# Optimization experiments

Measured on AMD Instinct MI355X. Metric: run time of the kernel, lower is better.

Reference implementation:

```python
import jax, jax.numpy as jnp
import numpy as np

B, S, D, H = 2, 2048, 1024, 16
DK = D // H
EPS = 1e-5


def setup_inputs() -> dict:
    key = jax.random.key(0)
    ks = jax.random.split(key, 6)
    std = (2.0 / (D + D)) ** 0.5
    return {
        "x": jax.random.normal(ks[0], (B, S, D), dtype=jnp.float32),
        "W_Q": jax.random.normal(ks[1], (D, D), dtype=jnp.float32) * std,
        "W_K": jax.random.normal(ks[2], (D, D), dtype=jnp.float32) * std,
        "W_V": jax.random.normal(ks[3], (D, D), dtype=jnp.float32) * std,
        "W_O": jax.random.normal(ks[4], (D, D), dtype=jnp.float32) * std,
        "gain": jnp.ones((D,), dtype=jnp.float32),
        "positions": jnp.arange(S, dtype=jnp.int64 if jax.config.jax_enable_x64 else jnp.int32),
        "theta": 10000,
        "max_seq_len": 2048,
    }


def rmsnorm(x, gain):
    xf = x.astype(jnp.float32)
    rms = jnp.sqrt(jnp.mean(xf * xf, axis=-1, keepdims=True) + EPS)
    return ((xf / rms) * gain).astype(x.dtype)


def apply_rope(x, sin, cos):
    # x: [..., seq, dk]; sin/cos: [seq, dk//2] broadcast over leading dims
    x_even = x[..., 0::2]
    x_odd = x[..., 1::2]
    r_even = x_even * cos - x_odd * sin
    r_odd = x_odd * cos + x_even * sin
    return jnp.stack([r_even, r_odd], axis=-1).reshape(x.shape)


def reference(x, W_Q, W_K, W_V, W_O, gain, positions, theta, max_seq_len):
    seq_len = x.shape[-2]
    Q = jnp.einsum('od,bsd->bso', W_Q, x)
    K = jnp.einsum('od,bsd->bso', W_K, x)
    V = jnp.einsum('od,bsd->bso', W_V, x)
    # RMSNorm over full d_model BEFORE head split (as in original)
    Q = rmsnorm(Q, gain)
    K = rmsnorm(K, gain)
    # split heads: [b, h, s, dk]
    Q = Q.reshape(*Q.shape[:-1], H, DK).swapaxes(-3, -2)
    K = K.reshape(*K.shape[:-1], H, DK).swapaxes(-3, -2)
    V = V.reshape(*V.shape[:-1], H, DK).swapaxes(-3, -2)
    # RoPE tables
    exponents = 2.0 * jnp.arange(DK // 2, dtype=jnp.float32) / DK
    inv_freq = 1.0 / (jnp.float32(theta) ** exponents)
    angles = positions.astype(jnp.float32)[:, None] * inv_freq[None, :]  # [S, DK//2]
    sin, cos = jnp.sin(angles), jnp.cos(angles)
    Q = apply_rope(Q, sin, cos)
    K = apply_rope(K, sin, cos)
    # causal attention
    scores = jnp.einsum('bhqd,bhkd->bhqk', Q, K) / jnp.sqrt(jnp.float32(DK))
    causal = jnp.tril(jnp.ones((seq_len, seq_len), dtype=bool))
    scores = jnp.where(causal, scores, -jnp.inf)
    attn = jax.nn.softmax(scores, axis=-1)
    out = jnp.einsum('bhqk,bhkd->bhqd', attn, V)
    out = out.swapaxes(-3, -2).reshape(*x.shape[:-1], D)
    return jnp.einsum('of,bsf->bso', W_O, out)
```

## Files before the change

### kernel.cpp

```cpp
#include <hip/hip_runtime.h>
#include <hip/hip_bf16.h>

typedef __attribute__((ext_vector_type(8))) __bf16 bf16x8;
typedef __attribute__((ext_vector_type(4))) __bf16 bf16x4;
typedef __attribute__((ext_vector_type(4))) float  f32x4;
typedef __attribute__((ext_vector_type(4))) short  s16x4;

#define S_LEN 2048
#define D_DIM 1024
#define NH    16
#define GK    1024
#define GN    1024

__device__ __forceinline__ float fast_exp2(float x) {
#if __has_builtin(__builtin_amdgcn_exp2f)
  return __builtin_amdgcn_exp2f(x);
#else
  return exp2f(x);
#endif
}

__device__ __forceinline__ f32x4 mfma16(bf16x4 a, bf16x4 b, f32x4 c) {
#if __has_builtin(__builtin_amdgcn_mfma_f32_16x16x16_bf16)
  return __builtin_amdgcn_mfma_f32_16x16x16_bf16(a, b, c, 0, 0, 0);
#else
  return __builtin_amdgcn_mfma_f32_16x16x16bf16_1k(
      __builtin_bit_cast(s16x4, a), __builtin_bit_cast(s16x4, b), c, 0, 0, 0);
#endif
}

__device__ __forceinline__ void gld_lds16(const void* g, void* l) {
  __builtin_amdgcn_global_load_lds(
      (const __attribute__((address_space(1))) unsigned int*)g,
      (__attribute__((address_space(3))) unsigned int*)l, 16, 0, 0);
}

__global__ __launch_bounds__(256) void cast_all(
    const float* __restrict__ x,  const float* __restrict__ wq, const float* __restrict__ wk,
    const float* __restrict__ wv, const float* __restrict__ wo,
    __bf16* __restrict__ xb, __bf16* __restrict__ wqb, __bf16* __restrict__ wkb,
    __bf16* __restrict__ wvb, __bf16* __restrict__ wob)
{
  const int NTOT = 2 << 20;
  for (int i = blockIdx.x * 256 + threadIdx.x; i < NTOT; i += 1024 * 256) {
    const float* s; __bf16* d; int off;
    if (i < (1 << 20)) { s = x; d = xb; off = i; }
    else {
      const int j = i - (1 << 20);
      const int r = j >> 18; off = j & ((1 << 18) - 1);
      s = (r == 0) ? wq : (r == 1) ? wk : (r == 2) ? wv : wo;
      d = (r == 0) ? wqb : (r == 1) ? wkb : (r == 2) ? wvb : wob;
    }
    float4 v = ((const float4*)s)[off];
    bf16x4 o = { (__bf16)v.x, (__bf16)v.y, (__bf16)v.z, (__bf16)v.w };
    ((bf16x4*)d)[off] = o;
  }
}

__global__ __launch_bounds__(256, 3) void gemm_qkv(
    const __bf16* __restrict__ A,
    const __bf16* __restrict__ W0, const __bf16* __restrict__ W1, const __bf16* __restrict__ W2,
    __bf16* __restrict__ C0, __bf16* __restrict__ C1, __bf16* __restrict__ VtOut)
{
  const int bid = blockIdx.x;
  const int e = bid & 7, mg = e >> 1, ng = e & 1;
  const int q = bid >> 3;
  const int mt = mg * 8 + (q & 7);
  const int nt = ng * 12 + (q >> 3);
  const int mode = nt >> 3;
  const int m0 = mt * 128;
  const int n0 = (nt & 7) * 128;
  const __bf16* Wm = (mode == 0) ? W0 : (mode == 1) ? W1 : W2;

  __shared__ __align__(16) __bf16 As[128 * 64];
  __shared__ __align__(16) __bf16 Bs[128 * 64];

  const int tid  = threadIdx.x;
  const int lane = tid & 63;
  const int w    = tid >> 6;
  const int wr   = w >> 1, wc = w & 1;
  const int lm   = lane & 15, qd = lane >> 4;

  const __bf16* ap[4]; int loA[4];
  #pragma unroll
  for (int j = 0; j < 4; j++) {
    const int c = tid + 256 * j;
    const int r = c >> 3, cpos = c & 7;
    ap[j] = A + (size_t)(m0 + r) * GK + (cpos ^ (r & 7)) * 8;
    loA[j] = c * 8;
  }
  const __bf16* bp[4]; int loB[4];
  #pragma unroll
  for (int j = 0; j < 4; j++) {
    const int c = tid + 256 * j;
    const int r = c >> 3, cpos = c & 7;
    bp[j] = Wm + (size_t)(n0 + r) * GK + (cpos ^ (r & 7)) * 8;
    loB[j] = c * 8;
  }

  const int sw = lm & 7;

  f32x4 zero = {0.f, 0.f, 0.f, 0.f};
  f32x4 acc[4][4];
  #pragma unroll
  for (int i = 0; i < 4; i++)
    #pragma unroll
    for (int j = 0; j < 4; j++) acc[i][j] = zero;

  for (int k0 = 0; k0 < GK; k0 += 64) {
    #pragma unroll
    for (int j = 0; j < 4; j++) gld_lds16(ap[j] + k0, &As[loA[j]]);
    #pragma unroll
    for (int j = 0; j < 4; j++) gld_lds16(bp[j] + k0, &Bs[loB[j]]);
    __syncthreads();
    #pragma unroll
    for (int half = 0; half < 2; half++) {
      const int cph = ((qd + 4 * half) ^ sw) * 8;
      bf16x8 af[4], bfv[4];
      #pragma unroll
      for (int i = 0; i < 4; i++) af[i]  = *(const bf16x8*)&As[(wr * 64 + i * 16 + lm) * 64 + cph];
      #pragma unroll
      for (int j = 0; j < 4; j++) bfv[j] = *(const bf16x8*)&Bs[(wc * 64 + j * 16 + lm) * 64 + cph];
      #pragma unroll
      for (int i = 0; i < 4; i++)
        #pragma unroll
        for (int j = 0; j < 4; j++)
          acc[i][j] = __builtin_amdgcn_mfma_f32_16x16x32_bf16(af[i], bfv[j], acc[i][j], 0, 0, 0);
    }
    __syncthreads();
  }

  if (mode < 2) {
    __bf16* C = (mode == 0) ? C0 : C1;
    #pragma unroll
    for (int i = 0; i < 4; i++) {
      const int row = m0 + wr * 64 + i * 16 + qd * 4;
      #pragma unroll
      for (int j = 0; j < 4; j++) {
        const int col = n0 + wc * 64 + j * 16 + lm;
        #pragma unroll
        for (int r = 0; r < 4; r++)
          C[(size_t)(row + r) * GN + col] = (__bf16)acc[i][j][r];
      }
    }
  } else {
    #pragma unroll
    for (int i = 0; i < 4; i++) {
      const int row = m0 + wr * 64 + i * 16 + qd * 4;
      const int b = row >> 11, s = row & (S_LEN - 1);
      #pragma unroll
      for (int j = 0; j < 4; j++) {
        const int col = n0 + wc * 64 + j * 16 + lm;
        const int h = col >> 6, d = col & 63;
        bf16x4 o = { (__bf16)acc[i][j][0], (__bf16)acc[i][j][1],
                     (__bf16)acc[i][j][2], (__bf16)acc[i][j][3] };
        *(bf16x4*)(VtOut + (((size_t)(b * NH + h) * 64 + d) * S_LEN + s)) = o;
      }
    }
  }
}

__global__ __launch_bounds__(256, 2) void gemm_out64(
    const __bf16* __restrict__ A, const __bf16* __restrict__ Wm, float* __restrict__ C)
{
  const int bid = blockIdx.x;
  const int e = bid & 7, mg = e >> 1, ng = e & 1;
  const int q = bid >> 3;
  const int m0 = (mg * 16 + (q & 15)) * 64;
  const int n0 = (ng * 4 + (q >> 4)) * 128;

  __shared__ __align__(16) __bf16 As[2][64 * 64];
  __shared__ __align__(16) __bf16 Bs[2][128 * 64];

  const int tid  = threadIdx.x;
  const int lane = tid & 63;
  const int w    = tid >> 6;
  const int wr   = w >> 1, wc = w & 1;
  const int lm   = lane & 15, qd = lane >> 4;

  const __bf16* ap[2]; int loA[2];
  #pragma unroll
  for (int j = 0; j < 2; j++) {
    const int c = tid + 256 * j;
    const int r = c >> 3, cpos = c & 7;
    ap[j] = A + (size_t)(m0 + r) * GK + (cpos ^ (r & 7)) * 8;
    loA[j] = c * 8;
  }
  const __bf16* bp[4]; int loB[4];
  #pragma unroll
  for (int j = 0; j < 4; j++) {
    const int c = tid + 256 * j;
    const int r = c >> 3, cpos = c & 7;
    bp[j] = Wm + (size_t)(n0 + r) * GK + (cpos ^ (r & 7)) * 8;
    loB[j] = c * 8;
  }

  const int sw = lm & 7;

  auto stage = [&](int buf, int k0) {
    #pragma unroll
    for (int j = 0; j < 2; j++) gld_lds16(ap[j] + k0, &As[buf][loA[j]]);
    #pragma unroll
    for (int j = 0; j < 4; j++) gld_lds16(bp[j] + k0, &Bs[buf][loB[j]]);
  };

  f32x4 zero = {0.f, 0.f, 0.f, 0.f};
  f32x4 acc[2][4];
  #pragma unroll
  for (int i = 0; i < 2; i++)
    #pragma unroll
    for (int j = 0; j < 4; j++) acc[i][j] = zero;

  stage(0, 0);

  for (int kt = 0; kt < 16; ++kt) {
    const int cur = kt & 1;
    __syncthreads();
    if (kt < 15) stage(cur ^ 1, (kt + 1) * 64);
    #pragma unroll
    for (int half = 0; half < 2; half++) {
      const int cph = ((qd + 4 * half) ^ sw) * 8;
      bf16x8 af[2], bfv[4];
      #pragma unroll
      for (int i = 0; i < 2; i++) af[i]  = *(const bf16x8*)&As[cur][(wr * 32 + i * 16 + lm) * 64 + cph];
      #pragma unroll
      for (int j = 0; j < 4; j++) bfv[j] = *(const bf16x8*)&Bs[cur][(wc * 64 + j * 16 + lm) * 64 + cph];
      #pragma unroll
      for (int i = 0; i < 2; i++)
        #pragma unroll
        for (int j = 0; j < 4; j++)
          acc[i][j] = __builtin_amdgcn_mfma_f32_16x16x32_bf16(af[i], bfv[j], acc[i][j], 0, 0, 0);
    }
  }

  #pragma unroll
  for (int i = 0; i < 2; i++) {
    const int row = m0 + wr * 32 + i * 16 + qd * 4;
    #pragma unroll
    for (int j = 0; j < 4; j++) {
      const int col = n0 + wc * 64 + j * 16 + lm;
      #pragma unroll
      for (int r = 0; r < 4; r++)
        C[(size_t)(row + r) * GN + col] = acc[i][j][r];
    }
  }
}

__global__ __launch_bounds__(256) void norm_rope(
    const __bf16* __restrict__ Qf, const __bf16* __restrict__ Kf,
    const float* __restrict__ gain, const int* __restrict__ positions,
    const int* __restrict__ theta_p,
    __bf16* __restrict__ Qh, __bf16* __restrict__ Kh)
{
  const int row = blockIdx.x;
  const int s = row & (S_LEN - 1), b = row >> 11;
  const int t = threadIdx.x, d0 = t * 4;

  const bf16x4 qv = *(const bf16x4*)(Qf + (size_t)row * D_DIM + d0);
  const bf16x4 kv = *(const bf16x4*)(Kf + (size_t)row * D_DIM + d0);
  const float q0 = (float)qv[0], q1 = (float)qv[1], q2 = (float)qv[2], q3 = (float)qv[3];
  const float k0 = (float)kv[0], k1 = (float)kv[1], k2 = (float)kv[2], k3 = (float)kv[3];

  float sq = q0 * q0 + q1 * q1 + q2 * q2 + q3 * q3;
  float sk = k0 * k0 + k1 * k1 + k2 * k2 + k3 * k3;
  #pragma unroll
  for (int off = 32; off; off >>= 1) { sq += __shfl_xor(sq, off); sk += __shfl_xor(sk, off); }
  __shared__ float red[8];
  const int lane = t & 63, wv = t >> 6;
  if (lane == 0) { red[wv] = sq; red[4 + wv] = sk; }
  __syncthreads();
  sq = red[0] + red[1] + red[2] + red[3];
  sk = red[4] + red[5] + red[6] + red[7];
  const float SC2 = 0.125f * 1.44269504089f;
  const float invq = rsqrtf(sq * (1.0f / 1024.0f) + 1e-5f) * SC2;
  const float invk = rsqrtf(sk * (1.0f / 1024.0f) + 1e-5f);

  const float4 g = *(const float4*)(gain + d0);
  const float qn0 = q0 * invq * g.x, qn1 = q1 * invq * g.y;
  const float qn2 = q2 * invq * g.z, qn3 = q3 * invq * g.w;
  const float kn0 = k0 * invk * g.x, kn1 = k1 * invk * g.y;
  const float kn2 = k2 * invk * g.z, kn3 = k3 * invk * g.w;

  const float pos = (float)positions[s];
  const float th  = (float)theta_p[0];
  const int idx = d0 & 63, h = d0 >> 6, p0 = idx >> 1;
  const float lg32 = __log2f(th) * (1.0f / 32.0f);
  const float f0 = fast_exp2(-(float)p0 * lg32);
  const float f1 = fast_exp2(-(float)(p0 + 1) * lg32);
  float s0, cc0, s1, cc1;
  __sincosf(pos * f0, &s0, &cc0);
  __sincosf(pos * f1, &s1, &cc1);

  const float qe0 = qn0 * cc0 - qn1 * s0, qo0 = qn1 * cc0 + qn0 * s0;
  const float qe1 = qn2 * cc1 - qn3 * s1, qo1 = qn3 * cc1 + qn2 * s1;
  const float ke0 = kn0 * cc0 - kn1 * s0, ko0 = kn1 * cc0 + kn0 * s0;
  const float ke1 = kn2 * cc1 - kn3 * s1, ko1 = kn3 * cc1 + kn2 * s1;

  const size_t obase = ((size_t)((b * NH + h) * S_LEN + s)) * 64 + idx;
  bf16x4 qo = { (__bf16)qe0, (__bf16)qo0, (__bf16)qe1, (__bf16)qo1 };
  bf16x4 ko = { (__bf16)ke0, (__bf16)ko0, (__bf16)ke1, (__bf16)ko1 };
  *(bf16x4*)(Qh + obase) = qo;
  *(bf16x4*)(Kh + obase) = ko;
}

__global__ __launch_bounds__(256) void attn_fwd(
    const __bf16* __restrict__ Qh, const __bf16* __restrict__ Kh,
    const __bf16* __restrict__ Vt, __bf16* __restrict__ Ob)
{
  const int bid = blockIdx.x;
  const int g   = bid >> 5;
  const int gj = g & 7, gs = g >> 3;
  const int qt  = gs ? gj : 15 - gj;
  const int rr  = bid & 31;
  const int bh  = (rr & 7) * 4 + (rr >> 3);
  const int tid = threadIdx.x, lane = tid & 63, w = tid >> 6;
  const int lm = lane & 15, qd = lane >> 4;

  __shared__ __align__(16) __bf16 smem[8192 + 8192];
  __bf16* Ks = smem;
  __bf16* Vs = smem + 8192;

  const int qA = qt * 128 + w * 32 + lm;
  const int qB = qA + 16;
  const size_t qbase = (size_t)bh * S_LEN * 64;
  const bf16x8 aqA0 = *(const bf16x8*)(Qh + qbase + (size_t)qA * 64 + qd * 8);
  const bf16x8 aqA1 = *(const bf16x8*)(Qh + qbase + (size_t)qA * 64 + 32 + qd * 8);
  const bf16x8 aqB0 = *(const bf16x8*)(Qh + qbase + (size_t)qB * 64 + qd * 8);
  const bf16x8 aqB1 = *(const bf16x8*)(Qh + qbase + (size_t)qB * 64 + 32 + qd * 8);

  const __bf16* Kb = Kh + (size_t)bh * S_LEN * 64;
  const __bf16* Vb = Vt + (size_t)bh * 64 * S_LEN;
  const int c0 = tid, c1 = 256 + tid;
  const int kr0 = c0 >> 3, kr1 = c1 >> 3;
  const int kg0 = ((c0 & 7) ^ (kr0 & 7)) * 8;
  const int kg1 = ((c1 & 7) ^ (kr1 & 7)) * 8;
  const int cpA = (qd ^ (lm & 7)) * 8;
  const int cpB = cpA ^ 32;

  auto stage = [&](int buf, int k0) {
    __bf16* Kd = Ks + buf * 4096;
    __bf16* Vd = Vs + buf * 4096;
    gld_lds16(Kb + (size_t)(k0 + kr0) * 64 + kg0, &Kd[c0 * 8]);
    gld_lds16(Kb + (size_t)(k0 + kr1) * 64 + kg1, &Kd[c1 * 8]);
    gld_lds16(Vb + (size_t)kr0 * S_LEN + k0 + kg0, &Vd[c0 * 8]);
    gld_lds16(Vb + (size_t)kr1 * S_LEN + k0 + kg1, &Vd[c1 * 8]);
  };

  f32x4 zero = {0.f, 0.f, 0.f, 0.f};
  f32x4 laccA = zero, laccB = zero;
  f32x4 oA[4], oB[4];
  #pragma unroll
  for (int jb = 0; jb < 4; jb++) { oA[jb] = zero; oB[jb] = zero; }

  bf16x4 ones4;
  #pragma unroll
  for (int i = 0; i < 4; i++) ones4[i] = (__bf16)1.0f;

  const int NT = 2 * qt + 2;
  const int wq0 = qt * 128 + w * 32;

  stage(0, 0);

  for (int kt = 0; kt < NT; ++kt) {
    const int cur = kt & 1;
    __syncthreads();
    if (kt < NT - 1) stage(cur ^ 1, (kt + 1) * 64);

    const int k0 = kt * 64;
    if (k0 > wq0 + 31) continue;

    const __bf16* Kc = Ks + cur * 4096;
    const __bf16* Vc = Vs + cur * 4096;
    const bool needMask = (k0 + 63 > wq0);

    bf16x4 pfA[4], pfB[4];
    #pragma unroll
    for (int kb = 0; kb < 4; kb++) {
      const int krow = (kb * 16 + lm) * 64;
      const bf16x8 ak0 = *(const bf16x8*)&Kc[krow + cpA];
      const bf16x8 ak1 = *(const bf16x8*)&Kc[krow + cpB];
      f32x4 scA = zero, scB = zero;
      scA = __builtin_amdgcn_mfma_f32_16x16x32_bf16(ak0, aqA0, scA, 0, 0, 0);
      scB = __builtin_amdgcn_mfma_f32_16x16x32_bf16(ak0, aqB0, scB, 0, 0, 0);
      scA = __builtin_amdgcn_mfma_f32_16x16x32_bf16(ak1, aqA1, scA, 0, 0, 0);
      scB = __builtin_amdgcn_mfma_f32_16x16x32_bf16(ak1, aqB1, scB, 0, 0, 0);
      float pA[4], pB[4];
      if (needMask) {
        const int keyb = k0 + kb * 16 + qd * 4;
        #pragma unroll
        for (int r = 0; r < 4; r++) {
          pA[r] = (keyb + r <= qA) ? fast_exp2(scA[r]) : 0.f;
          pB[r] = (keyb + r <= qB) ? fast_exp2(scB[r]) : 0.f;
        }
      } else {
        #pragma unroll
        for (int r = 0; r < 4; r++) { pA[r] = fast_exp2(scA[r]); pB[r] = fast_exp2(scB[r]); }
      }
      bf16x4 fA = { (__bf16)pA[0], (__bf16)pA[1], (__bf16)pA[2], (__bf16)pA[3] };
      bf16x4 fB = { (__bf16)pB[0], (__bf16)pB[1], (__bf16)pB[2], (__bf16)pB[3] };
      pfA[kb] = fA; pfB[kb] = fB;
      laccA = mfma16(ones4, fA, laccA);
      laccB = mfma16(ones4, fB, laccB);
    }

    #pragma unroll
    for (int jb = 0; jb < 4; jb++) {
      const int vrow = jb * 16 + lm;
      const int rsw = vrow & 7;
      #pragma unroll
      for (int kb = 0; kb < 4; kb++) {
        const int c = 2 * kb + (qd >> 1);
        const bf16x4 av = *(const bf16x4*)&Vc[vrow * 64 + ((c ^ rsw) << 3) + (qd & 1) * 4];
        oA[jb] = mfma16(av, pfA[kb], oA[jb]);
        oB[jb] = mfma16(av, pfB[kb], oB[jb]);
      }
    }
  }

  const int b = bh >> 4, h = bh & 15;
  const float invA = 1.0f / laccA[0];
  const float invB = 1.0f / laccB[0];
  const size_t baseA = ((size_t)(b * S_LEN + qA)) * D_DIM + h * 64 + qd * 4;
  const size_t baseB = baseA + (size_t)16 * D_DIM;
  #pragma unroll
  for (int jb = 0; jb < 4; jb++) {
    bf16x4 ovA = { (__bf16)(oA[jb][0] * invA), (__bf16)(oA[jb][1] * invA),
                   (__bf16)(oA[jb][2] * invA), (__bf16)(oA[jb][3] * invA) };
    bf16x4 ovB = { (__bf16)(oB[jb][0] * invB), (__bf16)(oB[jb][1] * invB),
                   (__bf16)(oB[jb][2] * invB), (__bf16)(oB[jb][3] * invB) };
    *(bf16x4*)(Ob + baseA + jb * 16) = ovA;
    *(bf16x4*)(Ob + baseB + jb * 16) = ovB;
  }
}

extern "C" void kernel_launch(void* const* d_in, const int* in_sizes, int n_in,
                              void* d_out, int out_size, void* d_ws, size_t ws_size,
                              hipStream_t stream)
{
  (void)in_sizes; (void)n_in; (void)out_size; (void)ws_size;
  const float* x    = (const float*)d_in[0];
  const float* WQ   = (const float*)d_in[1];
  const float* WK   = (const float*)d_in[2];
  const float* WV   = (const float*)d_in[3];
  const float* WO   = (const float*)d_in[4];
  const float* gain = (const float*)d_in[5];
  const int* positions = (const int*)d_in[6];
  const int* theta     = (const int*)d_in[7];
  float* out = (float*)d_out;

  char* ws = (char*)d_ws;
  const size_t MB = 1024 * 1024;
  __bf16* xb  = (__bf16*)(ws + 0);
  __bf16* WQb = (__bf16*)(ws + 8  * MB);
  __bf16* WKb = (__bf16*)(ws + 10 * MB);
  __bf16* WVb = (__bf16*)(ws + 12 * MB);
  __bf16* WOb = (__bf16*)(ws + 14 * MB);
  __bf16* Qfb = (__bf16*)(ws + 16 * MB);
  __bf16* Kfb = (__bf16*)(ws + 24 * MB);
  __bf16* Vt  = (__bf16*)(ws + 32 * MB);
  __bf16* Qh  = (__bf16*)(ws + 40 * MB);
  __bf16* Kh  = (__bf16*)(ws + 48 * MB);
  __bf16* Ob  = (__bf16*)(ws + 56 * MB);

  cast_all<<<1024, 256, 0, stream>>>(x, WQ, WK, WV, WO, xb, WQb, WKb, WVb, WOb);
  gemm_qkv<<<768, 256, 0, stream>>>(xb, WQb, WKb, WVb, Qfb, Kfb, Vt);
  norm_rope<<<4096, 256, 0, stream>>>(Qfb, Kfb, gain, positions, theta, Qh, Kh);
  attn_fwd<<<512, 256, 0, stream>>>(Qh, Kh, Vt, Ob);
  gemm_out64<<<512, 256, 0, stream>>>(Ob, WOb, out);
}
```

Baseline: 189.3 us.

## Replace LDS-staged K/V tiles with per-wave register loads and causal load balancing

Removes the shared-memory double buffer and the per-tile __syncthreads. Each wave now loads its K fragments directly from global memory into registers, double-buffered one tile ahead, and reads V fragments straight from global memory. Each wave owns a 32-query slot chosen so the four waves in a block get complementary causal lengths, and the block-to-head mapping is rearranged by XCD. It also asks for 2 blocks per CU through launch bounds. The cost is heavier register use and redundant global/L2 reads of K/V across waves, which were previously shared through LDS.

```diff
diff --git a/kernel.cpp b/kernel.cpp
--- a/kernel.cpp
+++ b/kernel.cpp
@@ -303,24 +303,26 @@
   *(bf16x4*)(Kh + obase) = ko;
 }
 
-__global__ __launch_bounds__(256) void attn_fwd(
+__global__ __launch_bounds__(256, 2) void attn_fwd(
     const __bf16* __restrict__ Qh, const __bf16* __restrict__ Kh,
     const __bf16* __restrict__ Vt, __bf16* __restrict__ Ob)
 {
   const int bid = blockIdx.x;
-  const int g   = bid >> 5;
-  const int gj = g & 7, gs = g >> 3;
-  const int qt  = gs ? gj : 15 - gj;
-  const int rr  = bid & 31;
-  const int bh  = (rr & 7) * 4 + (rr >> 3);
+  const int xcd = bid & 7;
+  const int t   = bid >> 3;
+  const int ib  = t & 15;
+  const int bh  = ((t >> 4) << 3) | xcd;
+
   const int tid = threadIdx.x, lane = tid & 63, w = tid >> 6;
   const int lm = lane & 15, qd = lane >> 4;
 
-  __shared__ __align__(16) __bf16 smem[8192 + 8192];
-  __bf16* Ks = smem;
-  __bf16* Vs = smem + 8192;
-
-  const int qA = qt * 128 + w * 32 + lm;
+  const int quant = (w + ib) & 3;
+  const int qslot = (quant == 0) ? ib : (quant == 1) ? 31 - ib
+                  : (quant == 2) ? 32 + ib : 63 - ib;
+  const int q0 = qslot * 32;
+  const int NT = (qslot >> 1) + 1;
+
+  const int qA = q0 + lm;
   const int qB = qA + 16;
   const size_t qbase = (size_t)bh * S_LEN * 64;
   const bf16x8 aqA0 = *(const bf16x8*)(Qh + qbase + (size_t)qA * 64 + qd * 8);
@@ -330,21 +332,6 @@
 
   const __bf16* Kb = Kh + (size_t)bh * S_LEN * 64;
   const __bf16* Vb = Vt + (size_t)bh * 64 * S_LEN;
-  const int c0 = tid, c1 = 256 + tid;
-  const int kr0 = c0 >> 3, kr1 = c1 >> 3;
-  const int kg0 = ((c0 & 7) ^ (kr0 & 7)) * 8;
-  const int kg1 = ((c1 & 7) ^ (kr1 & 7)) * 8;
-  const int cpA = (qd ^ (lm & 7)) * 8;
-  const int cpB = cpA ^ 32;
-
-  auto stage = [&](int buf, int k0) {
-    __bf16* Kd = Ks + buf * 4096;
-    __bf16* Vd = Vs + buf * 4096;
-    gld_lds16(Kb + (size_t)(k0 + kr0) * 64 + kg0, &Kd[c0 * 8]);
-    gld_lds16(Kb + (size_t)(k0 + kr1) * 64 + kg1, &Kd[c1 * 8]);
-    gld_lds16(Vb + (size_t)kr0 * S_LEN + k0 + kg0, &Vd[c0 * 8]);
-    gld_lds16(Vb + (size_t)kr1 * S_LEN + k0 + kg1, &Vd[c1 * 8]);
-  };
 
   f32x4 zero = {0.f, 0.f, 0.f, 0.f};
   f32x4 laccA = zero, laccB = zero;
@@ -356,66 +343,80 @@
   #pragma unroll
   for (int i = 0; i < 4; i++) ones4[i] = (__bf16)1.0f;
 
-  const int NT = 2 * qt + 2;
-  const int wq0 = qt * 128 + w * 32;
-
-  stage(0, 0);
-
+  bf16x8 kX0[4], kX1[4], kY0[4], kY1[4];
+
+#define LOADK(K0R, K1R, KT)                                                  \
+  {                                                                          \
+    const __bf16* kp_ = (KT);                                                \
+    _Pragma("unroll")                                                        \
+    for (int kb = 0; kb < 4; kb++) {                                         \
+      K0R[kb] = *(const bf16x8*)(kp_ + (size_t)(kb * 16 + lm) * 64 + qd * 8);       \
+      K1R[kb] = *(const bf16x8*)(kp_ + (size_t)(kb * 16 + lm) * 64 + 32 + qd * 8);  \
+    }                                                                        \
+  }
+
+#define TILE_BODY(K0R, K1R)                                                  \
+  {                                                                          \
+    const int k0 = kt << 6;                                                  \
+                           \
+    bf16x4 av[4][4];                                                         \
+    _Pragma("unroll")                                                        \
+    for (int jb = 0; jb < 4; jb++)                                           \
+      _Pragma("unroll")                                                      \
+      for (int kb = 0; kb < 4; kb++)                                         \
+        av[jb][kb] = *(const bf16x4*)(Vb + (size_t)(jb * 16 + lm) * S_LEN +  \
+                                      k0 + kb * 16 + qd * 4);                \
+    const bool needMask = (k0 + 63 > q0);                                    \
+    bf16x4 pfA[4], pfB[4];                                                   \
+    _Pragma("unroll")                                                        \
+    for (int kb = 0; kb < 4; kb++) {                                         \
+      f32x4 scA = zero, scB = zero;                                          \
+      scA = __builtin_amdgcn_mfma_f32_16x16x32_bf16(K0R[kb], aqA0, scA, 0, 0, 0); \
+      scB = __builtin_amdgcn_mfma_f32_16x16x32_bf16(K0R[kb], aqB0, scB, 0, 0, 0); \
+      scA = __builtin_amdgcn_mfma_f32_16x16x32_bf16(K1R[kb], aqA1, scA, 0, 0, 0); \
+      scB = __builtin_amdgcn_mfma_f32_16x16x32_bf16(K1R[kb], aqB1, scB, 0, 0, 0); \
+      float pA[4], pB[4];                                                    \
+      if (needMask) {                                                        \
+        const int keyb = k0 + kb * 16 + qd * 4;                              \
+        _Pragma("unroll")                                                    \
+        for (int r = 0; r < 4; r++) {                                        \
+          pA[r] = (keyb + r <= qA) ? fast_exp2(scA[r]) : 0.f;                \
+          pB[r] = (keyb + r <= qB) ? fast_exp2(scB[r]) : 0.f;                \
+        }                                                                    \
+      } else {                                                               \
+        _Pragma("unroll")                                                    \
+        for (int r = 0; r < 4; r++) {                                        \
+          pA[r] = fast_exp2(scA[r]); pB[r] = fast_exp2(scB[r]);              \
+        }                                                                    \
+      }                                                                      \
+      bf16x4 fA = { (__bf16)pA[0], (__bf16)pA[1], (__bf16)pA[2], (__bf16)pA[3] }; \
+      bf16x4 fB = { (__bf16)pB[0], (__bf16)pB[1], (__bf16)pB[2], (__bf16)pB[3] }; \
+      pfA[kb] = fA; pfB[kb] = fB;                                            \
+      laccA = mfma16(ones4, fA, laccA);                                      \
+      laccB = mfma16(ones4, fB, laccB);                                      \
+    }                                                                        \
+    _Pragma("unroll")                                                        \
+    for (int jb = 0; jb < 4; jb++)                                           \
+      _Pragma("unroll")                                                      \
+      for (int kb = 0; kb < 4; kb++) {                                       \
+        oA[jb] = mfma16(av[jb][kb], pfA[kb], oA[jb]);                        \
+        oB[jb] = mfma16(av[jb][kb], pfB[kb], oB[jb]);                        \
+      }                                                                      \
+  }
+
+  LOADK(kX0, kX1, Kb);
   for (int kt = 0; kt < NT; ++kt) {
-    const int cur = kt & 1;
-    __syncthreads();
-    if (kt < NT - 1) stage(cur ^ 1, (kt + 1) * 64);
-
-    const int k0 = kt * 64;
-    if (k0 > wq0 + 31) continue;
-
-    const __bf16* Kc = Ks + cur * 4096;
-    const __bf16* Vc = Vs + cur * 4096;
-    const bool needMask = (k0 + 63 > wq0);
-
-    bf16x4 pfA[4], pfB[4];
-    #pragma unroll
-    for (int kb = 0; kb < 4; kb++) {
-      const int krow = (kb * 16 + lm) * 64;
-      const bf16x8 ak0 = *(const bf16x8*)&Kc[krow + cpA];
-      const bf16x8 ak1 = *(const bf16x8*)&Kc[krow + cpB];
-      f32x4 scA = zero, scB = zero;
-      scA = __builtin_amdgcn_mfma_f32_16x16x32_bf16(ak0, aqA0, scA, 0, 0, 0);
-      scB = __builtin_amdgcn_mfma_f32_16x16x32_bf16(ak0, aqB0, scB, 0, 0, 0);
-      scA = __builtin_amdgcn_mfma_f32_16x16x32_bf16(ak1, aqA1, scA, 0, 0, 0);
-      scB = __builtin_amdgcn_mfma_f32_16x16x32_bf16(ak1, aqB1, scB, 0, 0, 0);
-      float pA[4], pB[4];
-      if (needMask) {
-        const int keyb = k0 + kb * 16 + qd * 4;
-        #pragma unroll
-        for (int r = 0; r < 4; r++) {
-          pA[r] = (keyb + r <= qA) ? fast_exp2(scA[r]) : 0.f;
-          pB[r] = (keyb + r <= qB) ? fast_exp2(scB[r]) : 0.f;
-        }
-      } else {
-        #pragma unroll
-        for (int r = 0; r < 4; r++) { pA[r] = fast_exp2(scA[r]); pB[r] = fast_exp2(scB[r]); }
-      }
-      bf16x4 fA = { (__bf16)pA[0], (__bf16)pA[1], (__bf16)pA[2], (__bf16)pA[3] };
-      bf16x4 fB = { (__bf16)pB[0], (__bf16)pB[1], (__bf16)pB[2], (__bf16)pB[3] };
-      pfA[kb] = fA; pfB[kb] = fB;
-      laccA = mfma16(ones4, fA, laccA);
-      laccB = mfma16(ones4, fB, laccB);
-    }
-
-    #pragma unroll
-    for (int jb = 0; jb < 4; jb++) {
-      const int vrow = jb * 16 + lm;
-      const int rsw = vrow & 7;
-      #pragma unroll
-      for (int kb = 0; kb < 4; kb++) {
-        const int c = 2 * kb + (qd >> 1);
-        const bf16x4 av = *(const bf16x4*)&Vc[vrow * 64 + ((c ^ rsw) << 3) + (qd & 1) * 4];
-        oA[jb] = mfma16(av, pfA[kb], oA[jb]);
-        oB[jb] = mfma16(av, pfB[kb], oB[jb]);
-      }
-    }
-  }
+    const __bf16* Knext = Kb + (size_t)((kt + 1) << 6) * 64;
+    if (kt & 1) {
+      if (kt + 1 < NT) LOADK(kX0, kX1, Knext);
+      TILE_BODY(kY0, kY1);
+    } else {
+      if (kt + 1 < NT) LOADK(kY0, kY1, Knext);
+      TILE_BODY(kX0, kX1);
+    }
+  }
+#undef LOADK
+#undef TILE_BODY
 
   const int b = bh >> 4, h = bh & 15;
   const float invA = 1.0f / laccA[0];
```

Result: slower. 234.4 us (+23.8%).
